# Optimization experiments

Measured on AMD Instinct MI355X. Metric: run time of the kernel, lower is better.

Reference implementation:

```python
import jax, jax.numpy as jnp
import numpy as np

S = 14          # grid size
L_COORD = 5.0
L_NOOBJ = 0.5
BATCH = 4096


def setup_inputs() -> dict:
    key = jax.random.key(0)
    k1, k2, k3 = jax.random.split(key, 3)
    shape = (BATCH, S, S, 30)
    # strictly positive values so sqrt(w), sqrt(h) are well defined (as assumed by the torch code)
    pred = jax.random.uniform(k1, shape, dtype=jnp.float32, minval=0.01, maxval=1.0)
    target = jax.random.uniform(k2, shape, dtype=jnp.float32, minval=0.01, maxval=1.0)
    has_obj = (jax.random.uniform(k3, (BATCH, S, S)) < 0.3).astype(jnp.float32)
    target = target.at[..., 4].set(has_obj)
    return {"pred_tensor": pred, "target_tensor": target}


def _yolo_loss(pred_tensor, target_tensor):
    N = pred_tensor.shape[0]
    dt = pred_tensor.dtype

    obj = (target_tensor[..., 4] > 0).astype(dt)      # [N,S,S]
    noobj = (target_tensor[..., 4] == 0).astype(dt)   # [N,S,S]

    # ---- no-object confidence loss (channels 4 and 9 in cells without objects) ----
    d4 = pred_tensor[..., 4] - target_tensor[..., 4]
    d9 = pred_tensor[..., 9] - target_tensor[..., 9]
    no_object_loss = jnp.sum(noobj * (d4 * d4 + d9 * d9))

    # ---- class prediction loss (channels 10:30 in object cells) ----
    dcls = pred_tensor[..., 10:] - target_tensor[..., 10:]
    class_loss = jnp.sum(obj[..., None] * dcls * dcls)

    # ---- per-cell best-IoU box selection (vectorized over all cells) ----
    pboxes = pred_tensor[..., :10].reshape(N, S, S, 2, 5)    # [N,S,S,2,5]
    tboxes = target_tensor[..., :10].reshape(N, S, S, 2, 5)
    p = pboxes[..., :4]                                      # [N,S,S,2,4]
    t = tboxes[..., 0, :4]                                   # target box of the cell [N,S,S,4]

    # [x,y,w,h] (center+size, xy in grid units) -> corner coords
    p1 = p[..., :2] / S - p[..., 2:] / 2                     # [N,S,S,2,2]
    p2 = p[..., :2] / S + p[..., 2:] / 2
    t1 = t[..., :2] / S - t[..., 2:] / 2                     # [N,S,S,2]
    t2 = t[..., :2] / S + t[..., 2:] / 2

    lt = jnp.maximum(p1, t1[..., None, :])
    rb = jnp.minimum(p2, t2[..., None, :])
    wh = jnp.maximum(rb - lt, 0.0)
    inter = wh[..., 0] * wh[..., 1]                          # [N,S,S,2]
    area_p = (p2[..., 0] - p1[..., 0]) * (p2[..., 1] - p1[..., 1])
    area_t = ((t2[..., 0] - t1[..., 0]) * (t2[..., 1] - t1[..., 1]))[..., None]
    iou = inter / (area_p + area_t - inter)                  # [N,S,S,2]

    # torch code: if IoU[0] > IoU[1] pick box 0 else box 1 (ties -> box 1)
    pick1 = iou[..., 0] <= iou[..., 1]                       # [N,S,S] bool
    p_sel = jnp.where(pick1[..., None], pboxes[..., 1, :], pboxes[..., 0, :])  # [N,S,S,5]
    t_sel = jnp.where(pick1[..., None], tboxes[..., 1, :], tboxes[..., 0, :])
    iou_best = jnp.where(pick1, iou[..., 1], iou[..., 0])    # [N,S,S]

    dxy = p_sel[..., :2] - t_sel[..., :2]
    dwh = jnp.sqrt(p_sel[..., 2:4]) - jnp.sqrt(t_sel[..., 2:4])
    reg_loss = jnp.sum(obj[..., None] * dxy * dxy) + jnp.sum(obj[..., None] * dwh * dwh)

    # ---- containing-object confidence loss: pred conf vs best IoU ----
    dconf = p_sel[..., 4] - iou_best
    contain_loss = jnp.sum(obj * dconf * dconf)

    total = L_NOOBJ * no_object_loss + class_loss + L_COORD * reg_loss + contain_loss
    return total / N


def reference(pred_tensor, target_tensor):
    return _yolo_loss(pred_tensor, target_tensor)
```

## Files before the change

### kernel.cpp

```cpp
#include <hip/hip_runtime.h>

#define SDIM 14
#define L_COORD 5.0f
#define L_NOOBJ 0.5f
#define BATCH 4096
#define CELLS (BATCH * SDIM * SDIM)
#define BLOCK 256
#define NBLOCKS (CELLS / BLOCK)
#define CELL_F 30

__global__ __launch_bounds__(BLOCK, 4) void yolo_partial(
    const float* __restrict__ pred, const float* __restrict__ targ,
    float* __restrict__ partial) {
    const int cell = blockIdx.x * BLOCK + threadIdx.x;
    const float* P = pred + (size_t)cell * CELL_F;
    const float* T = targ + (size_t)cell * CELL_F;

    float Pb[10], Tb[10];
#pragma unroll
    for (int j = 0; j < 5; ++j) {
        const float2 a = *reinterpret_cast<const float2*>(P + 2 * j);
        const float2 b = *reinterpret_cast<const float2*>(T + 2 * j);
        Pb[2 * j] = a.x; Pb[2 * j + 1] = a.y;
        Tb[2 * j] = b.x; Tb[2 * j + 1] = b.y;
    }

    float cls = 0.0f;
#pragma unroll
    for (int j = 5; j < 15; ++j) {
        const float2 a = *reinterpret_cast<const float2*>(P + 2 * j);
        const float2 b = *reinterpret_cast<const float2*>(T + 2 * j);
        const float dx = a.x - b.x;
        const float dy = a.y - b.y;
        cls += dx * dx;
        cls += dy * dy;
    }

    const float d4 = Pb[4] - Tb[4];
    const float d9 = Pb[9] - Tb[9];
    const float noobj_l = L_NOOBJ * (d4 * d4 + d9 * d9);

    const float invS = 1.0f / (float)SDIM;
    const float t1x = Tb[0] * invS - Tb[2] * 0.5f;
    const float t1y = Tb[1] * invS - Tb[3] * 0.5f;
    const float t2x = Tb[0] * invS + Tb[2] * 0.5f;
    const float t2y = Tb[1] * invS + Tb[3] * 0.5f;
    const float area_t = (t2x - t1x) * (t2y - t1y);

    float iou0 = 0.0f, iou1 = 0.0f;
#pragma unroll
    for (int k = 0; k < 2; ++k) {
        const float bx = Pb[5 * k + 0], by = Pb[5 * k + 1];
        const float bw = Pb[5 * k + 2], bh = Pb[5 * k + 3];
        const float p1x = bx * invS - bw * 0.5f;
        const float p1y = by * invS - bh * 0.5f;
        const float p2x = bx * invS + bw * 0.5f;
        const float p2y = by * invS + bh * 0.5f;
        const float ltx = fmaxf(p1x, t1x), lty = fmaxf(p1y, t1y);
        const float rbx = fminf(p2x, t2x), rby = fminf(p2y, t2y);
        const float wx = fmaxf(rbx - ltx, 0.0f);
        const float wy = fmaxf(rby - lty, 0.0f);
        const float inter = wx * wy;
        const float area_p = (p2x - p1x) * (p2y - p1y);
        const float v = inter / (area_p + area_t - inter);
        if (k == 0) iou0 = v; else iou1 = v;
    }

    const bool pick1 = (iou0 <= iou1);
    const float iou_best = pick1 ? iou1 : iou0;
    const float psx = pick1 ? Pb[5] : Pb[0];
    const float psy = pick1 ? Pb[6] : Pb[1];
    const float psw = pick1 ? Pb[7] : Pb[2];
    const float psh = pick1 ? Pb[8] : Pb[3];
    const float psc = pick1 ? Pb[9] : Pb[4];
    const float tsx = pick1 ? Tb[5] : Tb[0];
    const float tsy = pick1 ? Tb[6] : Tb[1];
    const float tsw = pick1 ? Tb[7] : Tb[2];
    const float tsh = pick1 ? Tb[8] : Tb[3];

    const float dx = psx - tsx, dy = psy - tsy;
    const float dw = sqrtf(psw) - sqrtf(tsw);
    const float dh = sqrtf(psh) - sqrtf(tsh);
    const float reg = dx * dx + dy * dy + dw * dw + dh * dh;
    const float dconf = psc - iou_best;
    const float obj_l = cls + L_COORD * reg + dconf * dconf;

    float loss = (Tb[4] > 0.0f) ? obj_l : noobj_l;

#pragma unroll
    for (int off = 32; off > 0; off >>= 1)
        loss += __shfl_down(loss, off, 64);

    __shared__ float wsum[BLOCK / 64];
    const int lane = threadIdx.x & 63;
    const int wave = threadIdx.x >> 6;
    if (lane == 0) wsum[wave] = loss;
    __syncthreads();
    if (threadIdx.x == 0)
        partial[blockIdx.x] = wsum[0] + wsum[1] + wsum[2] + wsum[3];
}

__global__ __launch_bounds__(BLOCK) void yolo_final(
    const float* __restrict__ partial, float* __restrict__ out) {
    float s = 0.0f;
    for (int i = threadIdx.x; i < NBLOCKS; i += BLOCK) s += partial[i];
#pragma unroll
    for (int off = 32; off > 0; off >>= 1)
        s += __shfl_down(s, off, 64);
    __shared__ float wsum[BLOCK / 64];
    const int lane = threadIdx.x & 63;
    const int wave = threadIdx.x >> 6;
    if (lane == 0) wsum[wave] = s;
    __syncthreads();
    if (threadIdx.x == 0)
        out[0] = (wsum[0] + wsum[1] + wsum[2] + wsum[3]) * (1.0f / (float)BATCH);
}

extern "C" void kernel_launch(void* const* d_in, const int* in_sizes, int n_in,
                              void* d_out, int out_size, void* d_ws, size_t ws_size,
                              hipStream_t stream) {
    const float* pred = (const float*)d_in[0];
    const float* targ = (const float*)d_in[1];
    float* out = (float*)d_out;
    float* partial = (float*)d_ws;

    yolo_partial<<<NBLOCKS, BLOCK, 0, stream>>>(pred, targ, partial);
    yolo_final<<<1, BLOCK, 0, stream>>>(partial, out);
}
```

Measured before the change: 209.0 us.

## Stage per-block cell data through LDS with coalesced float2 loads

Each thread previously read its own 30-float cell with strided float2 loads, so every wave instruction touched addresses spread across many cache lines. The block now loads its whole contiguous chunk of pred and target with fully coalesced float2 loads. It scatters box fields and precomputed class differences into shared memory, then each thread reads back its cell. Block size drops to 128, and the change adds an LDS round trip, a barrier, and likely bank conflicts from the stride-10/22 layout.

```diff
diff --git a/kernel.cpp b/kernel.cpp
--- a/kernel.cpp
+++ b/kernel.cpp
@@ -5,35 +5,68 @@
 #define L_NOOBJ 0.5f
 #define BATCH 4096
 #define CELLS (BATCH * SDIM * SDIM)
-#define BLOCK 256
+#define BLOCK 128
 #define NBLOCKS (CELLS / BLOCK)
 #define CELL_F 30
+#define BLK_F (BLOCK * CELL_F)
+#define BLK_F2 (BLK_F / 2)
+
+#define PBOX 0
+#define TBOX (BLOCK * 10)
+#define DCLS (2 * BLOCK * 10)
+#define WSUM (DCLS + BLOCK * 22)
+#define LDS_FLOATS (WSUM + 2)
 
 __global__ __launch_bounds__(BLOCK, 4) void yolo_partial(
     const float* __restrict__ pred, const float* __restrict__ targ,
     float* __restrict__ partial) {
-    const int cell = blockIdx.x * BLOCK + threadIdx.x;
-    const float* P = pred + (size_t)cell * CELL_F;
-    const float* T = targ + (size_t)cell * CELL_F;
+    __shared__ float lds[LDS_FLOATS];
+
+    const int tid = threadIdx.x;
+    const size_t base = (size_t)blockIdx.x * BLK_F;
+    const float* P = pred + base;
+    const float* T = targ + base;
+
+    float2 p2[15], t2[15];
+#pragma unroll
+    for (int j = 0; j < 15; ++j) {
+        const int idx = tid + j * BLOCK;
+        p2[j] = *reinterpret_cast<const float2*>(P + 2 * idx);
+        t2[j] = *reinterpret_cast<const float2*>(T + 2 * idx);
+    }
+
+#pragma unroll
+    for (int j = 0; j < 15; ++j) {
+        const int idx = tid + j * BLOCK;
+        const int cell = idx / 15;
+        const int c = (idx % 15) * 2;
+        if (c < 10) {
+            *reinterpret_cast<float2*>(&lds[PBOX + cell * 10 + c]) = p2[j];
+            *reinterpret_cast<float2*>(&lds[TBOX + cell * 10 + c]) = t2[j];
+        } else {
+            float2 d;
+            d.x = p2[j].x - t2[j].x;
+            d.y = p2[j].y - t2[j].y;
+            *reinterpret_cast<float2*>(&lds[DCLS + cell * 22 + (c - 10)]) = d;
+        }
+    }
+    __syncthreads();
 
     float Pb[10], Tb[10];
 #pragma unroll
     for (int j = 0; j < 5; ++j) {
-        const float2 a = *reinterpret_cast<const float2*>(P + 2 * j);
-        const float2 b = *reinterpret_cast<const float2*>(T + 2 * j);
+        const float2 a = *reinterpret_cast<const float2*>(&lds[PBOX + tid * 10 + 2 * j]);
+        const float2 b = *reinterpret_cast<const float2*>(&lds[TBOX + tid * 10 + 2 * j]);
         Pb[2 * j] = a.x; Pb[2 * j + 1] = a.y;
         Tb[2 * j] = b.x; Tb[2 * j + 1] = b.y;
     }
 
     float cls = 0.0f;
 #pragma unroll
-    for (int j = 5; j < 15; ++j) {
-        const float2 a = *reinterpret_cast<const float2*>(P + 2 * j);
-        const float2 b = *reinterpret_cast<const float2*>(T + 2 * j);
-        const float dx = a.x - b.x;
-        const float dy = a.y - b.y;
-        cls += dx * dx;
-        cls += dy * dy;
+    for (int j = 0; j < 10; ++j) {
+        const float2 d = *reinterpret_cast<const float2*>(&lds[DCLS + tid * 22 + 2 * j]);
+        cls += d.x * d.x;
+        cls += d.y * d.y;
     }
 
     const float d4 = Pb[4] - Tb[4];
@@ -91,23 +124,22 @@
     for (int off = 32; off > 0; off >>= 1)
         loss += __shfl_down(loss, off, 64);
 
-    __shared__ float wsum[BLOCK / 64];
-    const int lane = threadIdx.x & 63;
-    const int wave = threadIdx.x >> 6;
-    if (lane == 0) wsum[wave] = loss;
+    const int lane = tid & 63;
+    const int wave = tid >> 6;
+    if (lane == 0) lds[WSUM + wave] = loss;
     __syncthreads();
-    if (threadIdx.x == 0)
-        partial[blockIdx.x] = wsum[0] + wsum[1] + wsum[2] + wsum[3];
+    if (tid == 0)
+        partial[blockIdx.x] = lds[WSUM + 0] + lds[WSUM + 1];
 }
 
-__global__ __launch_bounds__(BLOCK) void yolo_final(
+__global__ __launch_bounds__(256) void yolo_final(
     const float* __restrict__ partial, float* __restrict__ out) {
     float s = 0.0f;
-    for (int i = threadIdx.x; i < NBLOCKS; i += BLOCK) s += partial[i];
+    for (int i = threadIdx.x; i < NBLOCKS; i += 256) s += partial[i];
 #pragma unroll
     for (int off = 32; off > 0; off >>= 1)
         s += __shfl_down(s, off, 64);
-    __shared__ float wsum[BLOCK / 64];
+    __shared__ float wsum[256 / 64];
     const int lane = threadIdx.x & 63;
     const int wave = threadIdx.x >> 6;
     if (lane == 0) wsum[wave] = s;
@@ -125,5 +157,5 @@
     float* partial = (float*)d_ws;
 
     yolo_partial<<<NBLOCKS, BLOCK, 0, stream>>>(pred, targ, partial);
-    yolo_final<<<1, BLOCK, 0, stream>>>(partial, out);
+    yolo_final<<<1, 256, 0, stream>>>(partial, out);
 }
```

New measurement: 211.1 us. Within noise of the previous version (+1.0%).
